# Optimization experiments

Hardware: AMD Instinct MI355X
Metric: run time of the kernel (lower is better)

The kernel has to match this reference:

```python
import jax, jax.numpy as jnp
import numpy as np

H_HEADS = 8

def _conv1x1(x, w):
    # x: (b, C_in, H, W), w: (C_out, C_in, 1, 1)
    return jax.lax.conv_general_dilated(
        x, w, window_strides=(1, 1), padding='VALID',
        dimension_numbers=('NCHW', 'OIHW', 'NCHW'))

def setup_inputs() -> dict:
    key = jax.random.key(0)
    kx, kq, kk, kv = jax.random.split(key, 4)
    x = jax.random.normal(kx, (16, 256, 64, 64), dtype=jnp.float32)
    sc = 1.0 / np.sqrt(256.0)
    wq = jax.random.normal(kq, (256, 256, 1, 1), dtype=jnp.float32) * sc
    wk = jax.random.normal(kk, (256, 256, 1, 1), dtype=jnp.float32) * sc
    wv = jax.random.normal(kv, (256, 256, 1, 1), dtype=jnp.float32) * sc
    return {"x": x, "wq": wq, "wk": wk, "wv": wv}

def reference(x, wq, wk, wv):
    b, _, Hs, Ws = x.shape
    h = H_HEADS
    v = _conv1x1(x, wv)                      # (b, C, H, W)
    C = v.shape[1]
    d = C // h
    q = _conv1x1(x, wq).reshape(b, h, d, -1)  # (b, h, d, N)
    k = _conv1x1(x, wk).reshape(b, h, d, -1)
    vflat = v.reshape(b, h, d, -1)
    # channel-attention: contract over spatial N -> (b, h, d, d)
    scores = jnp.einsum('bhdn,bhen->bhde', q, k) / jnp.sqrt(jnp.float32(h))
    attn_weights = jax.nn.softmax(scores, axis=-1)
    attn = jnp.einsum('bhde,bhen->bhdn', attn_weights, vflat)  # (b, h, d, N)
    # ChannelShuffle(groups=h): (b, h, d, H, W) -> (b, d, h, H, W) -> (b, C, H, W)
    shuffled = attn.reshape(b, h, d, Hs, Ws).transpose(0, 2, 1, 3, 4).reshape(b, C, Hs, Ws)
    out = shuffled + v
    return (out, attn_weights)
```

## Files before the change

### kernel.cpp

```cpp
#include <hip/hip_runtime.h>
#include <hip/hip_bf16.h>
#include <stdint.h>

typedef __attribute__((ext_vector_type(4))) float f32x4;
typedef __attribute__((ext_vector_type(8))) short bf16x8;
typedef __attribute__((ext_vector_type(4))) short bf16x4;
typedef __attribute__((ext_vector_type(4))) unsigned int u32x4;

__device__ __forceinline__ unsigned short f2bf_rne(float f) {
  union { float f; unsigned int u; } v; v.f = f;
  unsigned int r = v.u + 0x7FFFu + ((v.u >> 16) & 1u);
  return (unsigned short)(r >> 16);
}
__device__ __forceinline__ float bf2f(unsigned short s) {
  union { float f; unsigned int u; } v; v.u = ((unsigned int)s) << 16;
  return v.f;
}

__global__ __launch_bounds__(1024) void k_gram(const float* __restrict__ x,
                                               float* __restrict__ Gpart) {
  __shared__ __align__(16) unsigned char lds[2][32768];
  const int b = blockIdx.y;
  const int n0 = blockIdx.x << 8;
  const int t = threadIdx.x;
  const int lane = t & 63;
  const int w = t >> 6;
  const int wm = (w >> 2) << 6;
  const int wn = (w & 3) << 6;
  const int c_ld = t >> 2;
  const int noct = t & 3;
  const int lrow = lane & 15;
  const int lkg = lane >> 4;

  f32x4 acc[4][4];
#pragma unroll
  for (int i = 0; i < 4; i++)
#pragma unroll
    for (int j = 0; j < 4; j++) acc[i][j] = (f32x4){0.f, 0.f, 0.f, 0.f};

  const float* gx = x + (((size_t)(b * 256 + c_ld)) << 12) + n0 + (noct << 3);
  f32x4 v0 = *(const f32x4*)(gx);
  f32x4 v1 = *(const f32x4*)(gx + 4);

  for (int sub = 0; sub < 8; sub++) {
    unsigned char* buf = lds[sub & 1];
    float vv[8] = {v0[0], v0[1], v0[2], v0[3], v1[0], v1[1], v1[2], v1[3]};
    unsigned short hi[8], lo[8];
#pragma unroll
    for (int j = 0; j < 8; j++) {
      hi[j] = f2bf_rne(vv[j]);
      lo[j] = f2bf_rne(vv[j] - bf2f(hi[j]));
    }
    u32x4 hw = {(unsigned)hi[0] | ((unsigned)hi[1] << 16),
                (unsigned)hi[2] | ((unsigned)hi[3] << 16),
                (unsigned)hi[4] | ((unsigned)hi[5] << 16),
                (unsigned)hi[6] | ((unsigned)hi[7] << 16)};
    u32x4 lw = {(unsigned)lo[0] | ((unsigned)lo[1] << 16),
                (unsigned)lo[2] | ((unsigned)lo[3] << 16),
                (unsigned)lo[4] | ((unsigned)lo[5] << 16),
                (unsigned)lo[6] | ((unsigned)lo[7] << 16)};
    const int swz = (c_ld & 7) << 4;
    *(u32x4*)(buf + c_ld * 128 + (((noct << 4)) ^ swz)) = hw;
    *(u32x4*)(buf + c_ld * 128 + ((64 + (noct << 4)) ^ swz)) = lw;
    __syncthreads();

    if (sub < 7) {
      v0 = *(const f32x4*)(gx + ((sub + 1) << 5));
      v1 = *(const f32x4*)(gx + ((sub + 1) << 5) + 4);
    }

    bf16x8 bh[4], bl[4];
#pragma unroll
    for (int nf = 0; nf < 4; nf++) {
      int col = wn + (nf << 4) + lrow;
      int cs = (col & 7) << 4;
      bh[nf] = *(const bf16x8*)(buf + col * 128 + (((lkg << 4)) ^ cs));
      bl[nf] = *(const bf16x8*)(buf + col * 128 + ((64 + (lkg << 4)) ^ cs));
    }
#pragma unroll
    for (int mf = 0; mf < 4; mf++) {
      int row = wm + (mf << 4) + lrow;
      int rs = (row & 7) << 4;
      bf16x8 ah = *(const bf16x8*)(buf + row * 128 + (((lkg << 4)) ^ rs));
      bf16x8 al = *(const bf16x8*)(buf + row * 128 + ((64 + (lkg << 4)) ^ rs));
#pragma unroll
      for (int nf = 0; nf < 4; nf++) {
        acc[mf][nf] = __builtin_amdgcn_mfma_f32_16x16x32_bf16(ah, bh[nf], acc[mf][nf], 0, 0, 0);
        acc[mf][nf] = __builtin_amdgcn_mfma_f32_16x16x32_bf16(ah, bl[nf], acc[mf][nf], 0, 0, 0);
        acc[mf][nf] = __builtin_amdgcn_mfma_f32_16x16x32_bf16(al, bh[nf], acc[mf][nf], 0, 0, 0);
      }
    }
  }

  if (wm <= wn) {
    float* Gp = Gpart + (((size_t)(blockIdx.x * 16 + b)) << 16);
#pragma unroll
    for (int mf = 0; mf < 4; mf++)
#pragma unroll
      for (int nf = 0; nf < 4; nf++) {
        int col = wn + (nf << 4) + lrow;
#pragma unroll
        for (int r = 0; r < 4; r++) {
          int row = wm + (mf << 4) + (lkg << 2) + r;
          Gp[row * 256 + col] = acc[mf][nf][r];
        }
      }
  }
}

__global__ __launch_bounds__(1024) void k_reduce(const float* __restrict__ Gpart,
                                                 float* __restrict__ G) {
  __shared__ float tl[64][68];
  const int bx = blockIdx.x;
  const int b = bx / 10;
  const int tp = bx % 10;
  const int TI[10] = {0, 0, 0, 0, 1, 1, 1, 2, 2, 3};
  const int TJ[10] = {0, 1, 2, 3, 1, 2, 3, 2, 3, 3};
  const int i = TI[tp], j = TJ[tp];
  const int t = threadIdx.x;
  const int r = t >> 4, cq = t & 15;

  const float* src = Gpart + ((size_t)b << 16) + (size_t)(i * 64 + r) * 256 + j * 64 + (cq << 2);
  f32x4 s = *(const f32x4*)(src);
#pragma unroll
  for (int ch = 1; ch < 16; ch++)
    s += *(const f32x4*)(src + (((size_t)ch) << 20));
  *(f32x4*)(G + ((size_t)b << 16) + (size_t)(i * 64 + r) * 256 + j * 64 + (cq << 2)) = s;

  if (i != j) {
    *(f32x4*)&tl[r][cq << 2] = s;
    __syncthreads();
    const int c = t >> 4, q4 = t & 15;
    f32x4 m;
#pragma unroll
    for (int q = 0; q < 4; q++) m[q] = tl[(q4 << 2) + q][c];
    *(f32x4*)(G + ((size_t)b << 16) + (size_t)(j * 64 + c) * 256 + i * 64 + (q4 << 2)) = m;
  }
}

__global__ __launch_bounds__(512) void k_scores(const float* __restrict__ wq,
                                                const float* __restrict__ wk,
                                                const float* __restrict__ wv,
                                                const float* __restrict__ G,
                                                float* __restrict__ attn,
                                                unsigned short* __restrict__ Wout) {
  __shared__ float part[8][16][256];
  const int h = blockIdx.x, b = blockIdx.y, dg = blockIdx.z;
  const int t = threadIdx.x, lane = t & 63;
  const int wu = __builtin_amdgcn_readfirstlane(t >> 6);

  const float* wqrow = wq + (size_t)(h * 32 + dg * 16) * 256 + wu * 32;
  f32x4 tp[16];
#pragma unroll
  for (int d = 0; d < 16; d++) tp[d] = (f32x4){0.f, 0.f, 0.f, 0.f};

  const float* Gb = G + ((size_t)b << 16) + (size_t)(wu * 32) * 256 + (lane << 2);
  for (int s = 0; s < 32; s++) {
    f32x4 g = *(const f32x4*)(Gb + s * 256);
#pragma unroll
    for (int d = 0; d < 16; d++)
      tp[d] += g * wqrow[d * 256 + s];
  }
#pragma unroll
  for (int d = 0; d < 16; d++)
    *(f32x4*)&part[wu][d][lane << 2] = tp[d];
  __syncthreads();

#pragma unroll
  for (int u = 0; u < 2; u++) {
    int o = t * 2 + u;
    int d = o >> 6, q = (o & 63) << 2;
    f32x4 s = *(f32x4*)&part[0][d][q];
#pragma unroll
    for (int w2 = 1; w2 < 8; w2++) s += *(f32x4*)&part[w2][d][q];
    *(f32x4*)&part[0][d][q] = s;
  }
  __syncthreads();
  const float* Tb = &part[0][0][0];

  const int dls = t >> 5, es = t & 31;
  f32x4 sa = {0.f, 0.f, 0.f, 0.f};
  const float* Tr = Tb + dls * 256;
  const float* wkr = wk + (size_t)(h * 32 + es) * 256;
  for (int c4 = 0; c4 < 64; c4++)
    sa += *(const f32x4*)(Tr + (c4 << 2)) * *(const f32x4*)(wkr + (c4 << 2));
  float s = (sa[0] + sa[1] + sa[2] + sa[3]) * 0.35355339059327379f;

  float m = s;
#pragma unroll
  for (int off = 1; off < 32; off <<= 1) m = fmaxf(m, __shfl_xor(m, off));
  float p = expf(s - m);
  float su = p;
#pragma unroll
  for (int off = 1; off < 32; off <<= 1) su += __shfl_xor(su, off);
  float a = p / su;
  attn[(((b * 8 + h) * 32) + dg * 16 + dls) * 32 + es] = a;

  f32x4 o0 = {0.f, 0.f, 0.f, 0.f}, o1 = {0.f, 0.f, 0.f, 0.f};
  const float* wvh = wv + (size_t)(h * 32) * 256 + (lane << 2);
#pragma unroll
  for (int e = 0; e < 32; e++) {
    float a0 = __shfl(a, e);
    float a1 = __shfl(a, 32 + e);
    f32x4 vv = *(const f32x4*)(wvh + e * 256);
    o0 += vv * a0;
    o1 += vv * a1;
  }
  const int d0 = dg * 16 + 2 * wu;
  const int co0 = d0 * 8 + h, co1 = (d0 + 1) * 8 + h;
  o0 += *(const f32x4*)(wv + (size_t)co0 * 256 + (lane << 2));
  o1 += *(const f32x4*)(wv + (size_t)co1 * 256 + (lane << 2));
  bf16x4 p0, p1;
#pragma unroll
  for (int j = 0; j < 4; j++) {
    p0[j] = (short)f2bf_rne(o0[j]);
    p1[j] = (short)f2bf_rne(o1[j]);
  }
  *(bf16x4*)(Wout + ((size_t)(b * 256 + co0) << 8) + (lane << 2)) = p0;
  *(bf16x4*)(Wout + ((size_t)(b * 256 + co1) << 8) + (lane << 2)) = p1;
}

__global__ __launch_bounds__(512) void k_out(const float* __restrict__ x,
                                             const unsigned short* __restrict__ Wout,
                                             float* __restrict__ out) {
  __shared__ __align__(16) unsigned short Bt[2][4096];
  const int b = blockIdx.y;
  const int nb = blockIdx.x << 7;
  const int t = threadIdx.x;
  const int lane = t & 63;
  const int w = t >> 6;
  const int wm = (w >> 1) << 6;
  const int wn = (w & 1) << 6;
  const int lrow = lane & 15;
  const int lkg = lane >> 4;

  f32x4 acc[4][4];
#pragma unroll
  for (int i = 0; i < 4; i++)
#pragma unroll
    for (int j = 0; j < 4; j++) acc[i][j] = (f32x4){0.f, 0.f, 0.f, 0.f};

  const int pos = lane >> 3;
  const int cblk = 2 * (pos & 3) + (pos >> 2);
  const int ctil = cblk * 4 + ((lane & 7) >> 1);
  const int noff = (lane & 1) << 3;
  const float* gxb = x + (((size_t)b) << 20) + (size_t)ctil * 4096 + nb + (w << 4) + noff;
  const unsigned int bt0 = (unsigned int)(uintptr_t)(&Bt[0][0]);

  f32x4 xa = *(const f32x4*)(gxb);
  f32x4 xb = *(const f32x4*)(gxb + 4);

  for (int kt = 0; kt < 8; kt++) {
    const int p = kt & 1;
    bf16x8 pk;
#pragma unroll
    for (int j = 0; j < 4; j++) {
      pk[j] = (short)f2bf_rne(xa[j]);
      pk[4 + j] = (short)f2bf_rne(xb[j]);
    }
    *(bf16x8*)(&Bt[p][(w << 9) + (lane << 3)]) = pk;
    __syncthreads();

    if (kt < 7) {
      const float* nx = gxb + (((size_t)(kt + 1)) << 17);
      xa = *(const f32x4*)(nx);
      xb = *(const f32x4*)(nx + 4);
    }

    bf16x8 afr[4];
    const unsigned short* wrow = Wout + (((size_t)(b * 256)) << 8) + kt * 32 + (lkg << 3);
#pragma unroll
    for (int mf = 0; mf < 4; mf++) {
      int co = wm + (mf << 4) + lrow;
      afr[mf] = *(const bf16x8*)(wrow + ((size_t)co << 8));
    }

    bf16x4 t0[4], t1[4];
#pragma unroll
    for (int nf = 0; nf < 4; nf++) {
      unsigned int base = bt0 + (unsigned int)(p << 13) +
                          (unsigned int)((((wn >> 4) + nf)) << 10) + (lane << 3);
      asm volatile("ds_read_b64_tr_b16 %0, %1" : "=v"(t0[nf]) : "v"(base) : "memory");
      asm volatile("ds_read_b64_tr_b16 %0, %1 offset:512" : "=v"(t1[nf]) : "v"(base) : "memory");
    }
    asm volatile("s_waitcnt lgkmcnt(0)" ::: "memory");
    __builtin_amdgcn_sched_barrier(0);

    bf16x8 bfr[4];
#pragma unroll
    for (int nf = 0; nf < 4; nf++) {
      bfr[nf][0] = t0[nf][0]; bfr[nf][1] = t0[nf][1];
      bfr[nf][2] = t0[nf][2]; bfr[nf][3] = t0[nf][3];
      bfr[nf][4] = t1[nf][0]; bfr[nf][5] = t1[nf][1];
      bfr[nf][6] = t1[nf][2]; bfr[nf][7] = t1[nf][3];
    }
#pragma unroll
    for (int mf = 0; mf < 4; mf++)
#pragma unroll
      for (int nf = 0; nf < 4; nf++)
        acc[mf][nf] = __builtin_amdgcn_mfma_f32_16x16x32_bf16(afr[mf], bfr[nf], acc[mf][nf], 0, 0, 0);
  }

  float* ob = out + (((size_t)b) << 20) + nb;
#pragma unroll
  for (int mf = 0; mf < 4; mf++)
#pragma unroll
    for (int nf = 0; nf < 4; nf++) {
      int col = wn + (nf << 4) + lrow;
#pragma unroll
      for (int r = 0; r < 4; r++) {
        int row = wm + (mf << 4) + (lkg << 2) + r;
        ob[((size_t)row << 12) + col] = acc[mf][nf][r];
      }
    }
}

extern "C" void kernel_launch(void* const* d_in, const int* in_sizes, int n_in,
                              void* d_out, int out_size, void* d_ws, size_t ws_size,
                              hipStream_t stream) {
  const float* x = (const float*)d_in[0];
  const float* wq = (const float*)d_in[1];
  const float* wk = (const float*)d_in[2];
  const float* wv = (const float*)d_in[3];
  float* out = (float*)d_out;
  float* attn = out + (size_t)16 * 256 * 4096;

  float* Gpart = out;

  char* ws = (char*)d_ws;
  float* G = (float*)ws;
  unsigned short* Wout = (unsigned short*)(ws + (4 << 20));

  k_gram<<<dim3(16, 16), dim3(1024), 0, stream>>>(x, Gpart);
  k_reduce<<<dim3(160), dim3(1024), 0, stream>>>(Gpart, G);
  k_scores<<<dim3(8, 16, 2), dim3(512), 0, stream>>>(wq, wk, wv, G, attn, Wout);
  k_out<<<dim3(32, 16), dim3(512), 0, stream>>>(x, Wout, out);
}
```

Baseline: 102.6 us.

## Split gram blocks by output row half and shrink reduce blocks for more parallelism

The gram kernel now launches 512-thread blocks, each computing half of the 256x256 output tile rows, which doubles the grid to 512 blocks. Each block still loads the full x tile, and the load is re-mapped so each thread handles 16 contiguous floats. The register prefetch of the next sub-tile is dropped. The reduce kernel is split into 4x more 256-thread blocks, each handling 16 rows. This aims to raise occupancy and CU coverage, but doubles x reads and bf16 hi/lo conversion work in gram and loses the load/compute overlap.

```diff
diff --git a/kernel.cpp b/kernel.cpp
--- a/kernel.cpp
+++ b/kernel.cpp
@@ -17,18 +17,21 @@
   return v.f;
 }
 
-__global__ __launch_bounds__(1024) void k_gram(const float* __restrict__ x,
-                                               float* __restrict__ Gpart) {
+__global__ __launch_bounds__(512, 4) void k_gram(const float* __restrict__ x,
+                                                 float* __restrict__ Gpart) {
   __shared__ __align__(16) unsigned char lds[2][32768];
   const int b = blockIdx.y;
   const int n0 = blockIdx.x << 8;
+  const int half = blockIdx.z;
   const int t = threadIdx.x;
   const int lane = t & 63;
   const int w = t >> 6;
-  const int wm = (w >> 2) << 6;
-  const int wn = (w & 3) << 6;
-  const int c_ld = t >> 2;
-  const int noct = t & 3;
+  const int ti = (half << 1) + (w >> 2);
+  const int tj = w & 3;
+  const int wm = ti << 6;
+  const int wn = tj << 6;
+  const int row_ld = t >> 1;
+  const int nh = t & 1;
   const int lrow = lane & 15;
   const int lkg = lane >> 4;
 
@@ -38,36 +41,45 @@
 #pragma unroll
     for (int j = 0; j < 4; j++) acc[i][j] = (f32x4){0.f, 0.f, 0.f, 0.f};
 
-  const float* gx = x + (((size_t)(b * 256 + c_ld)) << 12) + n0 + (noct << 3);
-  f32x4 v0 = *(const f32x4*)(gx);
-  f32x4 v1 = *(const f32x4*)(gx + 4);
+  const float* gx = x + (((size_t)(b * 256 + row_ld)) << 12) + n0 + (nh << 4);
 
   for (int sub = 0; sub < 8; sub++) {
     unsigned char* buf = lds[sub & 1];
-    float vv[8] = {v0[0], v0[1], v0[2], v0[3], v1[0], v1[1], v1[2], v1[3]};
-    unsigned short hi[8], lo[8];
-#pragma unroll
-    for (int j = 0; j < 8; j++) {
+    f32x4 v0 = *(const f32x4*)(gx + (sub << 5));
+    f32x4 v1 = *(const f32x4*)(gx + (sub << 5) + 4);
+    f32x4 v2 = *(const f32x4*)(gx + (sub << 5) + 8);
+    f32x4 v3 = *(const f32x4*)(gx + (sub << 5) + 12);
+    float vv[16] = {v0[0], v0[1], v0[2], v0[3], v1[0], v1[1], v1[2], v1[3],
+                    v2[0], v2[1], v2[2], v2[3], v3[0], v3[1], v3[2], v3[3]};
+    unsigned short hi[16], lo[16];
+#pragma unroll
+    for (int j = 0; j < 16; j++) {
       hi[j] = f2bf_rne(vv[j]);
       lo[j] = f2bf_rne(vv[j] - bf2f(hi[j]));
     }
-    u32x4 hw = {(unsigned)hi[0] | ((unsigned)hi[1] << 16),
-                (unsigned)hi[2] | ((unsigned)hi[3] << 16),
-                (unsigned)hi[4] | ((unsigned)hi[5] << 16),
-                (unsigned)hi[6] | ((unsigned)hi[7] << 16)};
-    u32x4 lw = {(unsigned)lo[0] | ((unsigned)lo[1] << 16),
-                (unsigned)lo[2] | ((unsigned)lo[3] << 16),
-                (unsigned)lo[4] | ((unsigned)lo[5] << 16),
-                (unsigned)lo[6] | ((unsigned)lo[7] << 16)};
-    const int swz = (c_ld & 7) << 4;
-    *(u32x4*)(buf + c_ld * 128 + (((noct << 4)) ^ swz)) = hw;
-    *(u32x4*)(buf + c_ld * 128 + ((64 + (noct << 4)) ^ swz)) = lw;
+    u32x4 hw0 = {(unsigned)hi[0] | ((unsigned)hi[1] << 16),
+                 (unsigned)hi[2] | ((unsigned)hi[3] << 16),
+                 (unsigned)hi[4] | ((unsigned)hi[5] << 16),
+                 (unsigned)hi[6] | ((unsigned)hi[7] << 16)};
+    u32x4 hw1 = {(unsigned)hi[8] | ((unsigned)hi[9] << 16),
+                 (unsigned)hi[10] | ((unsigned)hi[11] << 16),
+                 (unsigned)hi[12] | ((unsigned)hi[13] << 16),
+                 (unsigned)hi[14] | ((unsigned)hi[15] << 16)};
+    u32x4 lw0 = {(unsigned)lo[0] | ((unsigned)lo[1] << 16),
+                 (unsigned)lo[2] | ((unsigned)lo[3] << 16),
+                 (unsigned)lo[4] | ((unsigned)lo[5] << 16),
+                 (unsigned)lo[6] | ((unsigned)lo[7] << 16)};
+    u32x4 lw1 = {(unsigned)lo[8] | ((unsigned)lo[9] << 16),
+                 (unsigned)lo[10] | ((unsigned)lo[11] << 16),
+                 (unsigned)lo[12] | ((unsigned)lo[13] << 16),
+                 (unsigned)lo[14] | ((unsigned)lo[15] << 16)};
+    const int swz = (row_ld & 7) << 4;
+    unsigned char* rbase = buf + row_ld * 128;
+    *(u32x4*)(rbase + (((nh << 5)) ^ swz)) = hw0;
+    *(u32x4*)(rbase + (((nh << 5) + 16) ^ swz)) = hw1;
+    *(u32x4*)(rbase + ((64 + (nh << 5)) ^ swz)) = lw0;
+    *(u32x4*)(rbase + ((64 + (nh << 5) + 16) ^ swz)) = lw1;
     __syncthreads();
-
-    if (sub < 7) {
-      v0 = *(const f32x4*)(gx + ((sub + 1) << 5));
-      v1 = *(const f32x4*)(gx + ((sub + 1) << 5) + 4);
-    }
 
     bf16x8 bh[4], bl[4];
 #pragma unroll
@@ -92,7 +104,7 @@
     }
   }
 
-  if (wm <= wn) {
+  if (tj >= ti) {
     float* Gp = Gpart + (((size_t)(blockIdx.x * 16 + b)) << 16);
 #pragma unroll
     for (int mf = 0; mf < 4; mf++)
@@ -108,33 +120,35 @@
   }
 }
 
-__global__ __launch_bounds__(1024) void k_reduce(const float* __restrict__ Gpart,
-                                                 float* __restrict__ G) {
-  __shared__ float tl[64][68];
+__global__ __launch_bounds__(256) void k_reduce(const float* __restrict__ Gpart,
+                                                float* __restrict__ G) {
+  __shared__ float tl[16][68];
   const int bx = blockIdx.x;
-  const int b = bx / 10;
-  const int tp = bx % 10;
+  const int b = bx / 40;
+  const int rem = bx % 40;
+  const int tp = rem >> 2, q = rem & 3;
   const int TI[10] = {0, 0, 0, 0, 1, 1, 1, 2, 2, 3};
   const int TJ[10] = {0, 1, 2, 3, 1, 2, 3, 2, 3, 3};
   const int i = TI[tp], j = TJ[tp];
   const int t = threadIdx.x;
   const int r = t >> 4, cq = t & 15;
-
-  const float* src = Gpart + ((size_t)b << 16) + (size_t)(i * 64 + r) * 256 + j * 64 + (cq << 2);
+  const int row = i * 64 + (q << 4) + r;
+
+  const float* src = Gpart + ((size_t)b << 16) + (size_t)row * 256 + j * 64 + (cq << 2);
   f32x4 s = *(const f32x4*)(src);
 #pragma unroll
   for (int ch = 1; ch < 16; ch++)
     s += *(const f32x4*)(src + (((size_t)ch) << 20));
-  *(f32x4*)(G + ((size_t)b << 16) + (size_t)(i * 64 + r) * 256 + j * 64 + (cq << 2)) = s;
+  *(f32x4*)(G + ((size_t)b << 16) + (size_t)row * 256 + j * 64 + (cq << 2)) = s;
 
   if (i != j) {
     *(f32x4*)&tl[r][cq << 2] = s;
     __syncthreads();
-    const int c = t >> 4, q4 = t & 15;
+    const int c = t >> 2, g = t & 3;
     f32x4 m;
 #pragma unroll
-    for (int q = 0; q < 4; q++) m[q] = tl[(q4 << 2) + q][c];
-    *(f32x4*)(G + ((size_t)b << 16) + (size_t)(j * 64 + c) * 256 + i * 64 + (q4 << 2)) = m;
+    for (int k = 0; k < 4; k++) m[k] = tl[(g << 2) + k][c];
+    *(f32x4*)(G + ((size_t)b << 16) + (size_t)(j * 64 + c) * 256 + i * 64 + (q << 4) + (g << 2)) = m;
   }
 }
 
@@ -331,8 +345,8 @@
   float* G = (float*)ws;
   unsigned short* Wout = (unsigned short*)(ws + (4 << 20));
 
-  k_gram<<<dim3(16, 16), dim3(1024), 0, stream>>>(x, Gpart);
-  k_reduce<<<dim3(160), dim3(1024), 0, stream>>>(Gpart, G);
+  k_gram<<<dim3(16, 16, 2), dim3(512), 0, stream>>>(x, Gpart);
+  k_reduce<<<dim3(640), dim3(256), 0, stream>>>(Gpart, G);
   k_scores<<<dim3(8, 16, 2), dim3(512), 0, stream>>>(wq, wk, wv, G, attn, Wout);
   k_out<<<dim3(32, 16), dim3(512), 0, stream>>>(x, Wout, out);
 }
```

Result: no change. 102.0 us (-0.6%).
